# Kernel optimization log

Hardware: AMD Instinct MI355X
Metric: run time of the kernel (lower is better)

Reference implementation:

```python
import jax, jax.numpy as jnp
import numpy as np

NODE_F = 8      # node_features
HID = 128       # hidden_dim
HEADS = 8       # nn.MultiheadAttention num_heads
OUT = 256       # output_dim
MAX_ATOMS = 4096  # max_pocket_atoms
NEIGHBOR_RADIUS = 3.0   # _compute_surface_scores neighbor_radius


def setup_inputs() -> dict:
    key = jax.random.key(0)
    ks = jax.random.split(key, 16)
    N, M = 16384, 32
    x = jax.random.normal(ks[0], (N, NODE_F), dtype=jnp.float32)
    pos = jax.random.normal(ks[1], (N, 3), dtype=jnp.float32) * 10.0
    ligand_pos = jax.random.normal(ks[2], (M, 3), dtype=jnp.float32) * 3.0

    def lin(k, fan_in, fan_out):
        return jax.random.normal(k, (fan_in, fan_out), dtype=jnp.float32) / np.sqrt(fan_in)

    return {
        'x': x, 'pos': pos, 'ligand_pos': ligand_pos,
        'W_node': lin(ks[3], NODE_F, HID), 'b_node': jnp.zeros((HID,), jnp.float32),
        'Wq': lin(ks[4], HID, HID), 'bq': jnp.zeros((HID,), jnp.float32),
        'Wk': lin(ks[5], HID, HID), 'bk': jnp.zeros((HID,), jnp.float32),
        'Wv': lin(ks[6], HID, HID), 'bv': jnp.zeros((HID,), jnp.float32),
        'Wo': lin(ks[7], HID, HID), 'bo': jnp.zeros((HID,), jnp.float32),
        'W1': lin(ks[8], HID, OUT), 'b1': jnp.zeros((OUT,), jnp.float32),
        'W2': lin(ks[9], OUT, OUT), 'b2': jnp.zeros((OUT,), jnp.float32),
    }


def _select_binding_site(pos, ligand_pos, k):
    # select_by_binding_site_proximity: distance-to-ligand-center + surface scores, topk
    lig_center = jnp.mean(ligand_pos, axis=0)                       # [3]
    d_lig = jnp.linalg.norm(pos - lig_center, axis=1)               # [N]
    # _compute_surface_scores: cdist(pos,pos) < 3.0, count neighbors (minus self)
    sq = jnp.sum(pos * pos, axis=1)                                 # [N]
    d2 = sq[:, None] + sq[None, :] - 2.0 * (pos @ pos.T)            # [N,N] squared distances
    neighbor_counts = jnp.sum(d2 < NEIGHBOR_RADIUS ** 2, axis=1) - 1
    surface = 1.0 / (neighbor_counts.astype(jnp.float32) + 1.0)
    scores = 1.0 / (1.0 + d_lig / 5.0) + 0.5 * surface
    _, idx = jax.lax.top_k(scores, k)                               # largest=True
    return idx


def reference(x, pos, ligand_pos, W_node, b_node, Wq, bq, Wk, bk, Wv, bv, Wo, bo, W1, b1, W2, b2):
    # N > max_pocket_atoms -> smart selection (adaptive with ligand_pos => binding_site)
    idx = _select_binding_site(pos, ligand_pos, MAX_ATOMS)
    xs = x[idx]                                                     # [K, NODE_F]

    # node embedding (E3 net call fails in the original -> h = node_embedding(x))
    h = xs @ W_node + b_node                                        # [K, HID]

    # MultiheadAttention over the single (batch=None) sequence, eval mode (no dropout)
    K = MAX_ATOMS
    dh = HID // HEADS
    q = (h @ Wq + bq).reshape(K, HEADS, dh).transpose(1, 0, 2)      # [H,K,dh]
    k_ = (h @ Wk + bk).reshape(K, HEADS, dh).transpose(1, 0, 2)
    v = (h @ Wv + bv).reshape(K, HEADS, dh).transpose(1, 0, 2)
    attn = jax.nn.softmax(jnp.einsum('hqd,hkd->hqk', q, k_) / np.sqrt(dh), axis=-1)
    av = jnp.einsum('hqk,hkd->hqd', attn, v).transpose(1, 0, 2).reshape(K, HID)
    h_att = av @ Wo + bo                                            # [K, HID]

    # global mean pool + output projection (Linear-ReLU-Linear)
    pooled = jnp.mean(h_att, axis=0)                                # [HID]
    out = jax.nn.relu(pooled @ W1 + b1) @ W2 + b2                   # [OUT]
    return out
```

## Files before the change

### kernel.cpp

```cpp
#include <hip/hip_runtime.h>
#include <cstdint>
#include <cstddef>

#define NPTS 16384
#define KSEL 4096
#define HIDDEN 128
#define NHEADS 8
#define DHEAD 16
#define OUTD 256
#define NSLICE 4

typedef __attribute__((ext_vector_type(8))) short bf16x8;
typedef __attribute__((ext_vector_type(4))) float f32x4;

#if defined(__has_builtin)
#if __has_builtin(__builtin_amdgcn_exp2f)
#define E2(x) __builtin_amdgcn_exp2f(x)
#endif
#endif
#ifndef E2
#define E2(x) exp2f(x)
#endif

constexpr size_t OFF_PX  = 1024;
constexpr size_t OFF_PY  = OFF_PX  + (size_t)NPTS*4;
constexpr size_t OFF_PZ  = OFF_PY  + (size_t)NPTS*4;
constexpr size_t OFF_SQ  = OFF_PZ  + (size_t)NPTS*4;
constexpr size_t OFF_DL  = OFF_SQ  + (size_t)NPTS*4;
constexpr size_t OFF_CNT = OFF_DL  + (size_t)NPTS*4;
constexpr size_t OFF_SEL = OFF_CNT + (size_t)NPTS*4;
constexpr size_t SZ_PK   = (size_t)NHEADS*KSEL*32*2;
constexpr size_t OFF_QPK = OFF_SEL + (size_t)KSEL*4;
constexpr size_t OFF_KPK = OFF_QPK + SZ_PK;
constexpr size_t OFF_V   = OFF_KPK + SZ_PK;
constexpr size_t OFF_LP  = OFF_V  + (size_t)KSEL*HIDDEN*4;
constexpr size_t OFF_RL  = OFF_LP + (size_t)NHEADS*KSEL*NSLICE*4;
constexpr size_t OFF_WP  = OFF_RL + (size_t)NHEADS*KSEL*4;
constexpr size_t OFF_PAV = OFF_WP + (size_t)NHEADS*KSEL*NSLICE*4;

__device__ __forceinline__ unsigned short f2bf(float f) {
    union { float f; unsigned u; } v; v.f = f;
    unsigned r = v.u + 0x7fffu + ((v.u >> 16) & 1u);
    return (unsigned short)(r >> 16);
}
__device__ __forceinline__ float bf2f(unsigned short h) {
    union { unsigned u; float f; } v; v.u = ((unsigned)h) << 16;
    return v.f;
}

__global__ void __launch_bounds__(256) k_prep(const float* __restrict__ pos, const float* __restrict__ lig, int M,
                       float* __restrict__ px, float* __restrict__ py, float* __restrict__ pz,
                       float* __restrict__ sq, float* __restrict__ dl) {
    __shared__ float ls[128];
    __shared__ float ctr[3];
    int tid = threadIdx.x;
    for (int i = tid; i < 3 * M; i += 256) ls[i] = lig[i];
    __syncthreads();
    if (tid < 3) {
        float s = 0.f;
        for (int i = 0; i < M; i++) s += ls[i * 3 + tid];
        ctr[tid] = s / (float)M;
    }
    __syncthreads();
    int i = blockIdx.x * 256 + tid;
    float x = pos[i*3+0], y = pos[i*3+1], z = pos[i*3+2];
    px[i] = x; py[i] = y; pz[i] = z;
    sq[i] = (x*x + y*y) + z*z;
    float dx = x - ctr[0], dy = y - ctr[1], dz = z - ctr[2];
    dl[i] = sqrtf((dx*dx + dy*dy) + dz*dz);
}

__global__ void __launch_bounds__(256) k_neighbor(const float* __restrict__ px, const float* __restrict__ py,
                                                  const float* __restrict__ pz, const float* __restrict__ sq,
                                                  int* __restrict__ cnt) {
    __shared__ float4 xt[128], yt[128], zt[128], st[128];
    int tid = threadIdx.x;
    int i = blockIdx.x * 256 + tid;
    float xi = px[i], yi = py[i], zi = pz[i], si = sq[i];
    int jbase = blockIdx.y * 512;
    if (tid < 128) {
        xt[tid] = ((const float4*)(px + jbase))[tid];
        yt[tid] = ((const float4*)(py + jbase))[tid];
        zt[tid] = ((const float4*)(pz + jbase))[tid];
        st[tid] = ((const float4*)(sq + jbase))[tid];
    }
    __syncthreads();
    int c = 0;
    for (int t = 0; t < 128; t++) {
        float4 xj = xt[t], yj = yt[t], zj = zt[t], sj = st[t];
        { float dot = fmaf(xi, xj.x, fmaf(yi, yj.x, zi*zj.x)); float d2 = (si + sj.x) - 2.0f*dot; c += (d2 < 9.0f); }
        { float dot = fmaf(xi, xj.y, fmaf(yi, yj.y, zi*zj.y)); float d2 = (si + sj.y) - 2.0f*dot; c += (d2 < 9.0f); }
        { float dot = fmaf(xi, xj.z, fmaf(yi, yj.z, zi*zj.z)); float d2 = (si + sj.z) - 2.0f*dot; c += (d2 < 9.0f); }
        { float dot = fmaf(xi, xj.w, fmaf(yi, yj.w, zi*zj.w)); float d2 = (si + sj.w) - 2.0f*dot; c += (d2 < 9.0f); }
    }
    atomicAdd(&cnt[i], c);
}

__global__ void __launch_bounds__(1024) k_select(const float* __restrict__ dl, const int* __restrict__ cnt,
                                                 int* __restrict__ sel) {
    __shared__ unsigned int sk[NPTS];
    __shared__ int hist[256];
    __shared__ unsigned int s_prefix;
    __shared__ int s_rem, s_eqtot, s_nout, s_digit, s_cgt;
    int tid = threadIdx.x;
    for (int i = tid; i < NPTS; i += 1024) {
        float score = 1.0f / (1.0f + dl[i] / 5.0f) + 0.5f * (1.0f / (float)cnt[i]);
        unsigned int u = __float_as_uint(score);
        sk[i] = u ^ ((u & 0x80000000u) ? 0xFFFFFFFFu : 0x80000000u);
    }
    if (tid == 0) { s_prefix = 0; s_rem = KSEL; s_nout = 0; s_eqtot = 0; }
    __syncthreads();
    for (int p = 0; p < 4; p++) {
        int sh = 24 - 8 * p;
        if (tid < 256) hist[tid] = 0;
        __syncthreads();
        unsigned int pref = s_prefix;
        int shp = (p == 0) ? 0 : (32 - 8 * p);
        for (int i = tid; i < NPTS; i += 1024) {
            unsigned int key = sk[i];
            bool m = (p == 0) || ((key >> shp) == pref);
            if (m) atomicAdd(&hist[(key >> sh) & 255], 1);
        }
        __syncthreads();
        int rem = s_rem;
        if (tid < 256) {
            int cg = 0;
            for (int d = tid + 1; d < 256; d++) cg += hist[d];
            if (cg < rem && cg + hist[tid] >= rem) { s_digit = tid; s_cgt = cg; }
        }
        __syncthreads();
        if (tid == 0) {
            s_prefix = (s_prefix << 8) | (unsigned int)s_digit;
            s_rem = rem - s_cgt;
            if (p == 3) s_eqtot = hist[s_digit];
        }
        __syncthreads();
    }
    unsigned int T = s_prefix;
    int need_eq = s_rem;
    for (int i = tid; i < NPTS; i += 1024)
        if (sk[i] > T) sel[atomicAdd(&s_nout, 1)] = i;
    __syncthreads();
    if (s_eqtot == need_eq) {
        for (int i = tid; i < NPTS; i += 1024)
            if (sk[i] == T) sel[atomicAdd(&s_nout, 1)] = i;
    } else {
        for (int i = tid; i < NPTS; i += 1024) {
            if (sk[i] == T) {
                int rank = 0;
                for (int j = 0; j < i; j++) rank += (sk[j] == T);
                if (rank < need_eq) sel[atomicAdd(&s_nout, 1)] = i;
            }
        }
    }
}

__device__ __forceinline__ void proj8(const float hs[8][HIDDEN], const float* __restrict__ W,
                                      float b, int d, float* acc) {
    #pragma unroll
    for (int r = 0; r < 8; r++) acc[r] = b;
    for (int c = 0; c < HIDDEN; c += 4) {
        float w0 = W[(c+0)*HIDDEN+d], w1 = W[(c+1)*HIDDEN+d], w2 = W[(c+2)*HIDDEN+d], w3 = W[(c+3)*HIDDEN+d];
        #pragma unroll
        for (int r = 0; r < 8; r++) {
            float4 h4 = *(const float4*)&hs[r][c];
            float a = acc[r];
            a = fmaf(h4.x, w0, a); a = fmaf(h4.y, w1, a); a = fmaf(h4.z, w2, a); a = fmaf(h4.w, w3, a);
            acc[r] = a;
        }
    }
}

__global__ void __launch_bounds__(128) k_qkv(const float* __restrict__ x, const int* __restrict__ sel,
        const float* __restrict__ Wn, const float* __restrict__ bn,
        const float* __restrict__ Wq, const float* __restrict__ bq,
        const float* __restrict__ Wk, const float* __restrict__ bk,
        const float* __restrict__ Wv, const float* __restrict__ bv,
        unsigned short* __restrict__ qpk, unsigned short* __restrict__ kpk,
        float* __restrict__ vg) {
    __shared__ float xs[8][8];
    __shared__ __align__(16) float hs[8][HIDDEN];
    int d = threadIdx.x;
    int r0 = blockIdx.x * 8;
    if (d < 64) { int rr = d >> 3, cc = d & 7; xs[rr][cc] = x[(size_t)sel[r0 + rr] * 8 + cc]; }
    __syncthreads();
    {
        float wn[8];
        #pragma unroll
        for (int c = 0; c < 8; c++) wn[c] = Wn[c * HIDDEN + d];
        float b = bn[d];
        #pragma unroll
        for (int r = 0; r < 8; r++) {
            float a = b;
            #pragma unroll
            for (int c = 0; c < 8; c++) a = fmaf(xs[r][c], wn[c], a);
            hs[r][d] = a;
        }
    }
    __syncthreads();
    int hh = d >> 4, dd = d & 15;
    float acc[8];
    proj8(hs, Wq, bq[d], d, acc);
    #pragma unroll
    for (int r = 0; r < 8; r++) {
        float val = acc[r] * 0.36067376022224085f;
        unsigned short hi = f2bf(val);
        unsigned short lo = f2bf(val - bf2f(hi));
        size_t idx = ((size_t)(hh * KSEL) + r0 + r) * 32 + dd;
        qpk[idx] = hi; qpk[idx + 16] = lo;
    }
    proj8(hs, Wk, bk[d], d, acc);
    #pragma unroll
    for (int r = 0; r < 8; r++) {
        float val = acc[r];
        unsigned short hi = f2bf(val);
        unsigned short lo = f2bf(val - bf2f(hi));
        size_t idx = ((size_t)(hh * KSEL) + r0 + r) * 32 + dd;
        kpk[idx] = hi; kpk[idx + 16] = lo;
    }
    proj8(hs, Wv, bv[d], d, acc);
    #pragma unroll
    for (int r = 0; r < 8; r++) vg[(size_t)(r0+r)*HIDDEN + d] = acc[r];
}

__global__ void __launch_bounds__(256) k_attn_l(
        const unsigned short* __restrict__ qpk, const unsigned short* __restrict__ kpk,
        float* __restrict__ lp) {
    __shared__ unsigned short smem[256 * 40];
    int tid = threadIdx.x;
    int ks = blockIdx.x, yg = blockIdx.y, h = blockIdx.z;
    size_t hb = (size_t)h * KSEL;
    int lane = tid & 63, w = tid >> 6;
    int n = lane & 15, g = lane >> 4;
    int q0w = yg * 64 + w * 16;
    bf16x8 afrag = *(const bf16x8*)(qpk + (hb + q0w + n) * 32 + g * 8);
    float l0 = 0.f, l1 = 0.f, l2 = 0.f, l3 = 0.f;
    int b1off = (g & 1) * 8;
    int b2off = 16 + g * 8;
    for (int kc = 0; kc < 4; kc++) {
        __syncthreads();
        {
            int krow = ks * 1024 + kc * 256 + tid;
            const float4* src = (const float4*)(kpk + (hb + krow) * 32);
            float4 a0 = src[0], a1 = src[1], a2 = src[2], a3 = src[3];
            float4* dst = (float4*)&smem[tid * 40];
            dst[0] = a0; dst[1] = a1; dst[2] = a2; dst[3] = a3;
        }
        __syncthreads();
        #pragma unroll 4
        for (int t = 0; t < 16; t++) {
            const unsigned short* rowp = &smem[(t * 16 + n) * 40];
            bf16x8 b1 = *(const bf16x8*)(rowp + b1off);
            bf16x8 b2 = {0,0,0,0,0,0,0,0};
            if (g < 2) b2 = *(const bf16x8*)(rowp + b2off);
            f32x4 c = {0.f, 0.f, 0.f, 0.f};
            c = __builtin_amdgcn_mfma_f32_16x16x32_bf16(afrag, b1, c, 0, 0, 0);
            c = __builtin_amdgcn_mfma_f32_16x16x32_bf16(afrag, b2, c, 0, 0, 0);
            l0 += E2(c[0]); l1 += E2(c[1]); l2 += E2(c[2]); l3 += E2(c[3]);
        }
    }
    #pragma unroll
    for (int m = 1; m < 16; m <<= 1) {
        l0 += __shfl_xor(l0, m); l1 += __shfl_xor(l1, m);
        l2 += __shfl_xor(l2, m); l3 += __shfl_xor(l3, m);
    }
    if (n == 0) {
        size_t base = (hb + q0w + g * 4) * NSLICE + ks;
        lp[base]            = l0; lp[base + NSLICE]     = l1;
        lp[base + 2*NSLICE] = l2; lp[base + 3*NSLICE]   = l3;
    }
}

__global__ void k_rl(const float* __restrict__ lp, float* __restrict__ rl) {
    int i = blockIdx.x * 256 + threadIdx.x;
    float4 p = ((const float4*)lp)[i];
    rl[i] = 1.0f / ((p.x + p.y) + (p.z + p.w));
}

__global__ void __launch_bounds__(256) k_attn_w(
        const unsigned short* __restrict__ qpk, const unsigned short* __restrict__ kpk,
        const float* __restrict__ rl, float* __restrict__ wp) {
    __shared__ unsigned short smem[256 * 40];
    __shared__ float rls[256];
    int tid = threadIdx.x;
    int qs = blockIdx.x, yg = blockIdx.y, h = blockIdx.z;
    size_t hb = (size_t)h * KSEL;
    int lane = tid & 63, w = tid >> 6;
    int n = lane & 15, g = lane >> 4;
    int j0w = yg * 64 + w * 16;
    bf16x8 afrag = *(const bf16x8*)(kpk + (hb + j0w + n) * 32 + g * 8);
    float w0 = 0.f, w1 = 0.f, w2 = 0.f, w3 = 0.f;
    int b1off = (g & 1) * 8;
    int b2off = 16 + g * 8;
    for (int qc = 0; qc < 4; qc++) {
        __syncthreads();
        {
            int qrow = qs * 1024 + qc * 256 + tid;
            const float4* src = (const float4*)(qpk + (hb + qrow) * 32);
            float4 a0 = src[0], a1 = src[1], a2 = src[2], a3 = src[3];
            float4* dst = (float4*)&smem[tid * 40];
            dst[0] = a0; dst[1] = a1; dst[2] = a2; dst[3] = a3;
            rls[tid] = rl[hb + qrow];
        }
        __syncthreads();
        #pragma unroll 4
        for (int t = 0; t < 16; t++) {
            const unsigned short* rowp = &smem[(t * 16 + n) * 40];
            bf16x8 b1 = *(const bf16x8*)(rowp + b1off);
            bf16x8 b2 = {0,0,0,0,0,0,0,0};
            if (g < 2) b2 = *(const bf16x8*)(rowp + b2off);
            f32x4 c = {0.f, 0.f, 0.f, 0.f};
            c = __builtin_amdgcn_mfma_f32_16x16x32_bf16(afrag, b1, c, 0, 0, 0);
            c = __builtin_amdgcn_mfma_f32_16x16x32_bf16(afrag, b2, c, 0, 0, 0);
            float rv = rls[t * 16 + n];
            w0 = fmaf(E2(c[0]), rv, w0); w1 = fmaf(E2(c[1]), rv, w1);
            w2 = fmaf(E2(c[2]), rv, w2); w3 = fmaf(E2(c[3]), rv, w3);
        }
    }
    #pragma unroll
    for (int m = 1; m < 16; m <<= 1) {
        w0 += __shfl_xor(w0, m); w1 += __shfl_xor(w1, m);
        w2 += __shfl_xor(w2, m); w3 += __shfl_xor(w3, m);
    }
    if (n == 0) {
        size_t base = (hb + j0w + g * 4) * NSLICE + qs;
        wp[base]            = w0; wp[base + NSLICE]     = w1;
        wp[base + 2*NSLICE] = w2; wp[base + 3*NSLICE]   = w3;
    }
}

__global__ void __launch_bounds__(256) k_colsum(const float* __restrict__ wp, const float* __restrict__ vg,
                                                float* __restrict__ pav) {
    __shared__ float wl[NHEADS][128];
    __shared__ float red[128];
    int tid = threadIdx.x;
    int jb = blockIdx.x * 128;
    for (int i = tid; i < NHEADS * 128; i += 256) {
        int h = i >> 7, jl = i & 127;
        float4 p = ((const float4*)wp)[(size_t)h * KSEL + jb + jl];
        wl[h][jl] = (p.x + p.y) + (p.z + p.w);
    }
    __syncthreads();
    int d = tid & 127, g = tid >> 7;
    int h = d >> 4;
    float acc = 0.f;
    for (int jl = g * 64; jl < g * 64 + 64; jl++)
        acc = fmaf(wl[h][jl], vg[(size_t)(jb + jl) * HIDDEN + d], acc);
    if (g == 1) red[d] = acc;
    __syncthreads();
    if (g == 0) atomicAdd(&pav[d], (acc + red[d]) * (1.0f / (float)KSEL));
}

__global__ void __launch_bounds__(256) k_final(const float* __restrict__ pav,
        const float* __restrict__ Wo, const float* __restrict__ bo,
        const float* __restrict__ W1, const float* __restrict__ b1,
        const float* __restrict__ W2, const float* __restrict__ b2,
        float* __restrict__ out) {
    __shared__ float sp[HIDDEN];
    __shared__ float st[OUTD];
    int t = threadIdx.x;
    if (t < HIDDEN) {
        float a = bo[t];
        for (int c = 0; c < HIDDEN; c++) a = fmaf(pav[c], Wo[c * HIDDEN + t], a);
        sp[t] = a;
    }
    __syncthreads();
    {
        float a = b1[t];
        for (int c = 0; c < HIDDEN; c++) a = fmaf(sp[c], W1[c * OUTD + t], a);
        st[t] = fmaxf(a, 0.f);
    }
    __syncthreads();
    {
        float o = b2[t];
        for (int c = 0; c < OUTD; c++) o = fmaf(st[c], W2[c * OUTD + t], o);
        out[t] = o;
    }
}

extern "C" void kernel_launch(void* const* d_in, const int* in_sizes, int n_in,
                              void* d_out, int out_size, void* d_ws, size_t ws_size,
                              hipStream_t stream) {
    (void)n_in; (void)out_size; (void)ws_size;
    const float* x   = (const float*)d_in[0];
    const float* pos = (const float*)d_in[1];
    const float* lig = (const float*)d_in[2];
    const float* Wn  = (const float*)d_in[3];
    const float* bn  = (const float*)d_in[4];
    const float* Wq  = (const float*)d_in[5];
    const float* bq  = (const float*)d_in[6];
    const float* Wk  = (const float*)d_in[7];
    const float* bk  = (const float*)d_in[8];
    const float* Wv  = (const float*)d_in[9];
    const float* bv  = (const float*)d_in[10];
    const float* Wo  = (const float*)d_in[11];
    const float* bo  = (const float*)d_in[12];
    const float* W1  = (const float*)d_in[13];
    const float* b1  = (const float*)d_in[14];
    const float* W2  = (const float*)d_in[15];
    const float* b2  = (const float*)d_in[16];
    int M = in_sizes[2] / 3;

    char* ws = (char*)d_ws;
    float*          px  = (float*)(ws + OFF_PX);
    float*          py  = (float*)(ws + OFF_PY);
    float*          pz  = (float*)(ws + OFF_PZ);
    float*          sq  = (float*)(ws + OFF_SQ);
    float*          dl  = (float*)(ws + OFF_DL);
    int*            cnt = (int*)  (ws + OFF_CNT);
    int*            sel = (int*)  (ws + OFF_SEL);
    unsigned short* qpk = (unsigned short*)(ws + OFF_QPK);
    unsigned short* kpk = (unsigned short*)(ws + OFF_KPK);
    float*          vg  = (float*)(ws + OFF_V);
    float*          lp  = (float*)(ws + OFF_LP);
    float*          rl  = (float*)(ws + OFF_RL);
    float*          wp  = (float*)(ws + OFF_WP);
    float*          pav = (float*)(ws + OFF_PAV);

    hipMemsetAsync(ws + OFF_CNT, 0, (size_t)NPTS * 4, stream);
    hipMemsetAsync(ws + OFF_PAV, 0, (size_t)HIDDEN * 4, stream);

    hipLaunchKernelGGL(k_prep,     dim3(64),       dim3(256),  0, stream, pos, lig, M, px, py, pz, sq, dl);
    hipLaunchKernelGGL(k_neighbor, dim3(64, 32),   dim3(256),  0, stream, px, py, pz, sq, cnt);
    hipLaunchKernelGGL(k_select,   dim3(1),        dim3(1024), 0, stream, dl, cnt, sel);
    hipLaunchKernelGGL(k_qkv,      dim3(KSEL/8),   dim3(128),  0, stream, x, sel, Wn, bn, Wq, bq, Wk, bk, Wv, bv, qpk, kpk, vg);
    hipLaunchKernelGGL(k_attn_l,   dim3(4, 64, 8), dim3(256),  0, stream, qpk, kpk, lp);
    hipLaunchKernelGGL(k_rl,       dim3(NHEADS*KSEL/256), dim3(256), 0, stream, lp, rl);
    hipLaunchKernelGGL(k_attn_w,   dim3(4, 64, 8), dim3(256),  0, stream, qpk, kpk, rl, wp);
    hipLaunchKernelGGL(k_colsum,   dim3(32),       dim3(256),  0, stream, wp, vg, pav);
    hipLaunchKernelGGL(k_final,    dim3(1),        dim3(256),  0, stream, pav, Wo, bo, W1, b1, W2, b2, (float*)d_out);
}
```

Before: 289.7 us.

## Compute pairwise neighbor counts with bf16 split MFMA plus exact fixup

Replaces the scalar FP32 all-pairs distance loop with MFMA 16x16x32 bf16 products, using a hi/lo bf16 split of coordinates to approximate -2·dot plus the squared norms. Pairs whose approximate distance lies within an error band of the radius threshold are appended to a flag list, and a new fixup kernel recomputes them exactly in FP32. The top-k digit search in the select kernel also swaps its per-thread O(256) suffix sum for a parallel scan. The risks are atomic contention on the flag counter and silent miscounts if more than the capped number of pairs are flagged or the error band is too tight.

```diff
diff --git a/kernel.cpp b/kernel.cpp
--- a/kernel.cpp
+++ b/kernel.cpp
@@ -9,6 +9,7 @@
 #define DHEAD 16
 #define OUTD 256
 #define NSLICE 4
+#define FCAP 131072
 
 typedef __attribute__((ext_vector_type(8))) short bf16x8;
 typedef __attribute__((ext_vector_type(4))) float f32x4;
@@ -22,21 +23,22 @@
 #define E2(x) exp2f(x)
 #endif
 
-constexpr size_t OFF_PX  = 1024;
-constexpr size_t OFF_PY  = OFF_PX  + (size_t)NPTS*4;
-constexpr size_t OFF_PZ  = OFF_PY  + (size_t)NPTS*4;
-constexpr size_t OFF_SQ  = OFF_PZ  + (size_t)NPTS*4;
-constexpr size_t OFF_DL  = OFF_SQ  + (size_t)NPTS*4;
-constexpr size_t OFF_CNT = OFF_DL  + (size_t)NPTS*4;
-constexpr size_t OFF_SEL = OFF_CNT + (size_t)NPTS*4;
-constexpr size_t SZ_PK   = (size_t)NHEADS*KSEL*32*2;
-constexpr size_t OFF_QPK = OFF_SEL + (size_t)KSEL*4;
-constexpr size_t OFF_KPK = OFF_QPK + SZ_PK;
-constexpr size_t OFF_V   = OFF_KPK + SZ_PK;
-constexpr size_t OFF_LP  = OFF_V  + (size_t)KSEL*HIDDEN*4;
-constexpr size_t OFF_RL  = OFF_LP + (size_t)NHEADS*KSEL*NSLICE*4;
-constexpr size_t OFF_WP  = OFF_RL + (size_t)NHEADS*KSEL*4;
-constexpr size_t OFF_PAV = OFF_WP + (size_t)NHEADS*KSEL*NSLICE*4;
+constexpr size_t OFF_PA    = 1024;
+constexpr size_t OFF_PB    = OFF_PA  + (size_t)NPTS*32;
+constexpr size_t OFF_SQ    = OFF_PB  + (size_t)NPTS*32;
+constexpr size_t OFF_DL    = OFF_SQ  + (size_t)NPTS*4;
+constexpr size_t OFF_CNT   = OFF_DL  + (size_t)NPTS*4;
+constexpr size_t OFF_NFLAG = OFF_CNT + (size_t)NPTS*4;
+constexpr size_t OFF_FLG   = OFF_NFLAG + 1024;
+constexpr size_t OFF_SEL   = OFF_FLG + (size_t)FCAP*4;
+constexpr size_t SZ_PK     = (size_t)NHEADS*KSEL*32*2;
+constexpr size_t OFF_QPK   = OFF_SEL + (size_t)KSEL*4;
+constexpr size_t OFF_KPK   = OFF_QPK + SZ_PK;
+constexpr size_t OFF_V     = OFF_KPK + SZ_PK;
+constexpr size_t OFF_LP    = OFF_V  + (size_t)KSEL*HIDDEN*4;
+constexpr size_t OFF_RL    = OFF_LP + (size_t)NHEADS*KSEL*NSLICE*4;
+constexpr size_t OFF_WP    = OFF_RL + (size_t)NHEADS*KSEL*4;
+constexpr size_t OFF_PAV   = OFF_WP + (size_t)NHEADS*KSEL*NSLICE*4;
 
 __device__ __forceinline__ unsigned short f2bf(float f) {
     union { float f; unsigned u; } v; v.f = f;
@@ -49,7 +51,7 @@
 }
 
 __global__ void __launch_bounds__(256) k_prep(const float* __restrict__ pos, const float* __restrict__ lig, int M,
-                       float* __restrict__ px, float* __restrict__ py, float* __restrict__ pz,
+                       unsigned short* __restrict__ pa, unsigned short* __restrict__ pb,
                        float* __restrict__ sq, float* __restrict__ dl) {
     __shared__ float ls[128];
     __shared__ float ctr[3];
@@ -64,42 +66,113 @@
     __syncthreads();
     int i = blockIdx.x * 256 + tid;
     float x = pos[i*3+0], y = pos[i*3+1], z = pos[i*3+2];
-    px[i] = x; py[i] = y; pz[i] = z;
     sq[i] = (x*x + y*y) + z*z;
     float dx = x - ctr[0], dy = y - ctr[1], dz = z - ctr[2];
     dl[i] = sqrtf((dx*dx + dy*dy) + dz*dz);
-}
-
-__global__ void __launch_bounds__(256) k_neighbor(const float* __restrict__ px, const float* __restrict__ py,
-                                                  const float* __restrict__ pz, const float* __restrict__ sq,
-                                                  int* __restrict__ cnt) {
-    __shared__ float4 xt[128], yt[128], zt[128], st[128];
+    unsigned short xh = f2bf(x); float xr = bf2f(xh); float xl = x - xr;
+    unsigned short yh = f2bf(y); float yr = bf2f(yh); float yl = y - yr;
+    unsigned short zh = f2bf(z); float zr = bf2f(zh); float zl = z - zr;
+    unsigned short xlb = f2bf(xl), ylb = f2bf(yl), zlb = f2bf(zl);
+    unsigned short xhA = f2bf(-2.f*xr), xlA = f2bf(-2.f*xl);
+    unsigned short yhA = f2bf(-2.f*yr), ylA = f2bf(-2.f*yl);
+    unsigned short zhA = f2bf(-2.f*zr), zlA = f2bf(-2.f*zl);
+    union { unsigned short s[16]; float4 f[2]; } A, B;
+    #pragma unroll
+    for (int t = 0; t < 16; t++) { A.s[t] = 0; B.s[t] = 0; }
+    A.s[0]=xhA; A.s[1]=xhA; A.s[2]=xlA;
+    A.s[3]=yhA; A.s[4]=yhA; A.s[5]=ylA;
+    A.s[6]=zhA; A.s[7]=zhA; A.s[8]=zlA;
+    A.s[9]=xlA; A.s[10]=ylA; A.s[11]=zlA;
+    B.s[0]=xh;  B.s[1]=xlb;  B.s[2]=xh;
+    B.s[3]=yh;  B.s[4]=ylb;  B.s[5]=yh;
+    B.s[6]=zh;  B.s[7]=zlb;  B.s[8]=zh;
+    B.s[9]=xlb; B.s[10]=ylb; B.s[11]=zlb;
+    float4* pad = (float4*)(pa + (size_t)i * 16);
+    pad[0] = A.f[0]; pad[1] = A.f[1];
+    float4* pbd = (float4*)(pb + (size_t)i * 16);
+    pbd[0] = B.f[0]; pbd[1] = B.f[1];
+}
+
+__global__ void __launch_bounds__(256) k_neighbor(
+        const unsigned short* __restrict__ pa, const unsigned short* __restrict__ pb,
+        const float* __restrict__ sq, int* __restrict__ cnt,
+        unsigned int* __restrict__ flg, unsigned int* __restrict__ nflag) {
+    __shared__ unsigned short bs[256 * 24];
+    __shared__ float sjs[256];
     int tid = threadIdx.x;
-    int i = blockIdx.x * 256 + tid;
-    float xi = px[i], yi = py[i], zi = pz[i], si = sq[i];
-    int jbase = blockIdx.y * 512;
-    if (tid < 128) {
-        xt[tid] = ((const float4*)(px + jbase))[tid];
-        yt[tid] = ((const float4*)(py + jbase))[tid];
-        zt[tid] = ((const float4*)(pz + jbase))[tid];
-        st[tid] = ((const float4*)(sq + jbase))[tid];
-    }
-    __syncthreads();
-    int c = 0;
-    for (int t = 0; t < 128; t++) {
-        float4 xj = xt[t], yj = yt[t], zj = zt[t], sj = st[t];
-        { float dot = fmaf(xi, xj.x, fmaf(yi, yj.x, zi*zj.x)); float d2 = (si + sj.x) - 2.0f*dot; c += (d2 < 9.0f); }
-        { float dot = fmaf(xi, xj.y, fmaf(yi, yj.y, zi*zj.y)); float d2 = (si + sj.y) - 2.0f*dot; c += (d2 < 9.0f); }
-        { float dot = fmaf(xi, xj.z, fmaf(yi, yj.z, zi*zj.z)); float d2 = (si + sj.z) - 2.0f*dot; c += (d2 < 9.0f); }
-        { float dot = fmaf(xi, xj.w, fmaf(yi, yj.w, zi*zj.w)); float d2 = (si + sj.w) - 2.0f*dot; c += (d2 < 9.0f); }
-    }
-    atomicAdd(&cnt[i], c);
+    int lane = tid & 63, w = tid >> 6;
+    int n = lane & 15, g = lane >> 4;
+    int i0 = blockIdx.x * 64 + w * 16;
+    bf16x8 afrag = {0,0,0,0,0,0,0,0};
+    if (g < 2) afrag = *(const bf16x8*)(pa + (size_t)(i0 + n) * 16 + g * 8);
+    int irow = i0 + g * 4;
+    float si0 = sq[irow+0], si1 = sq[irow+1], si2 = sq[irow+2], si3 = sq[irow+3];
+    int boff = (g < 2) ? g * 8 : 0;
+    int jb0 = blockIdx.y * 4096;
+    int c0 = 0, c1 = 0, c2 = 0, c3 = 0;
+    for (int ch = 0; ch < 16; ch++) {
+        __syncthreads();
+        int jb = jb0 + ch * 256;
+        {
+            const float4* src = (const float4*)(pb + (size_t)(jb + tid) * 16);
+            float4 v0 = src[0], v1 = src[1];
+            float4* dst = (float4*)&bs[tid * 24];
+            dst[0] = v0; dst[1] = v1;
+            sjs[tid] = sq[jb + tid];
+        }
+        __syncthreads();
+        #pragma unroll 4
+        for (int t = 0; t < 16; t++) {
+            int jj = t * 16 + n;
+            bf16x8 bfrag = *(const bf16x8*)&bs[jj * 24 + boff];
+            float sj = sjs[jj];
+            float s0 = si0 + sj, s1 = si1 + sj, s2 = si2 + sj, s3 = si3 + sj;
+            f32x4 c; c[0] = s0; c[1] = s1; c[2] = s2; c[3] = s3;
+            c = __builtin_amdgcn_mfma_f32_16x16x32_bf16(afrag, bfrag, c, 0, 0, 0);
+            float t0 = fmaf(s0, 3.0e-4f, 0.01f), t1 = fmaf(s1, 3.0e-4f, 0.01f);
+            float t2 = fmaf(s2, 3.0e-4f, 0.01f), t3 = fmaf(s3, 3.0e-4f, 0.01f);
+            float d0 = c[0] - 9.0f, d1 = c[1] - 9.0f, d2_ = c[2] - 9.0f, d3 = c[3] - 9.0f;
+            c0 += (d0 < -t0); c1 += (d1 < -t1); c2 += (d2_ < -t2); c3 += (d3 < -t3);
+            int j = jb + jj;
+            if (fabsf(d0) < t0) { unsigned idx = atomicAdd(nflag, 1u); if (idx < FCAP) flg[idx] = ((unsigned)(irow+0) << 14) | (unsigned)j; }
+            if (fabsf(d1) < t1) { unsigned idx = atomicAdd(nflag, 1u); if (idx < FCAP) flg[idx] = ((unsigned)(irow+1) << 14) | (unsigned)j; }
+            if (fabsf(d2_) < t2) { unsigned idx = atomicAdd(nflag, 1u); if (idx < FCAP) flg[idx] = ((unsigned)(irow+2) << 14) | (unsigned)j; }
+            if (fabsf(d3) < t3) { unsigned idx = atomicAdd(nflag, 1u); if (idx < FCAP) flg[idx] = ((unsigned)(irow+3) << 14) | (unsigned)j; }
+        }
+    }
+    #pragma unroll
+    for (int m = 1; m < 16; m <<= 1) {
+        c0 += __shfl_xor(c0, m); c1 += __shfl_xor(c1, m);
+        c2 += __shfl_xor(c2, m); c3 += __shfl_xor(c3, m);
+    }
+    if (n == 0) {
+        atomicAdd(&cnt[irow+0], c0);
+        atomicAdd(&cnt[irow+1], c1);
+        atomicAdd(&cnt[irow+2], c2);
+        atomicAdd(&cnt[irow+3], c3);
+    }
+}
+
+__global__ void __launch_bounds__(256) k_fixup(const float* __restrict__ pos, const float* __restrict__ sq,
+        const unsigned int* __restrict__ flg, const unsigned int* __restrict__ nflag,
+        int* __restrict__ cnt) {
+    int nf = (int)*nflag; if (nf > FCAP) nf = FCAP;
+    for (int idx = blockIdx.x * 256 + threadIdx.x; idx < nf; idx += gridDim.x * 256) {
+        unsigned pr = flg[idx];
+        int i = (int)(pr >> 14), j = (int)(pr & 16383u);
+        float xi = pos[i*3+0], yi = pos[i*3+1], zi = pos[i*3+2];
+        float xj = pos[j*3+0], yj = pos[j*3+1], zj = pos[j*3+2];
+        float dot = fmaf(xi, xj, fmaf(yi, yj, zi * zj));
+        float d2 = (sq[i] + sq[j]) - 2.0f * dot;
+        if (d2 < 9.0f) atomicAdd(&cnt[i], 1);
+    }
 }
 
 __global__ void __launch_bounds__(1024) k_select(const float* __restrict__ dl, const int* __restrict__ cnt,
                                                  int* __restrict__ sel) {
     __shared__ unsigned int sk[NPTS];
     __shared__ int hist[256];
+    __shared__ int scan2[256];
     __shared__ unsigned int s_prefix;
     __shared__ int s_rem, s_eqtot, s_nout, s_digit, s_cgt;
     int tid = threadIdx.x;
@@ -122,11 +195,20 @@
             if (m) atomicAdd(&hist[(key >> sh) & 255], 1);
         }
         __syncthreads();
+        if (tid < 256) scan2[tid] = hist[tid];
+        __syncthreads();
+        for (int off = 1; off < 256; off <<= 1) {
+            int v = 0;
+            if (tid < 256) { v = scan2[tid]; if (tid + off < 256) v += scan2[tid + off]; }
+            __syncthreads();
+            if (tid < 256) scan2[tid] = v;
+            __syncthreads();
+        }
         int rem = s_rem;
         if (tid < 256) {
-            int cg = 0;
-            for (int d = tid + 1; d < 256; d++) cg += hist[d];
-            if (cg < rem && cg + hist[tid] >= rem) { s_digit = tid; s_cgt = cg; }
+            int hi = scan2[tid];
+            int lo = hi - hist[tid];
+            if (hi >= rem && lo < rem) { s_digit = tid; s_cgt = lo; }
         }
         __syncthreads();
         if (tid == 0) {
@@ -402,12 +484,13 @@
     int M = in_sizes[2] / 3;
 
     char* ws = (char*)d_ws;
-    float*          px  = (float*)(ws + OFF_PX);
-    float*          py  = (float*)(ws + OFF_PY);
-    float*          pz  = (float*)(ws + OFF_PZ);
+    unsigned short* pa  = (unsigned short*)(ws + OFF_PA);
+    unsigned short* pb  = (unsigned short*)(ws + OFF_PB);
     float*          sq  = (float*)(ws + OFF_SQ);
     float*          dl  = (float*)(ws + OFF_DL);
     int*            cnt = (int*)  (ws + OFF_CNT);
+    unsigned int*   nfl = (unsigned int*)(ws + OFF_NFLAG);
+    unsigned int*   flg = (unsigned int*)(ws + OFF_FLG);
     int*            sel = (int*)  (ws + OFF_SEL);
     unsigned short* qpk = (unsigned short*)(ws + OFF_QPK);
     unsigned short* kpk = (unsigned short*)(ws + OFF_KPK);
@@ -417,11 +500,12 @@
     float*          wp  = (float*)(ws + OFF_WP);
     float*          pav = (float*)(ws + OFF_PAV);
 
-    hipMemsetAsync(ws + OFF_CNT, 0, (size_t)NPTS * 4, stream);
+    hipMemsetAsync(ws + OFF_CNT, 0, (size_t)NPTS * 4 + 1024, stream);
     hipMemsetAsync(ws + OFF_PAV, 0, (size_t)HIDDEN * 4, stream);
 
-    hipLaunchKernelGGL(k_prep,     dim3(64),       dim3(256),  0, stream, pos, lig, M, px, py, pz, sq, dl);
-    hipLaunchKernelGGL(k_neighbor, dim3(64, 32),   dim3(256),  0, stream, px, py, pz, sq, cnt);
+    hipLaunchKernelGGL(k_prep,     dim3(64),       dim3(256),  0, stream, pos, lig, M, pa, pb, sq, dl);
+    hipLaunchKernelGGL(k_neighbor, dim3(256, 4),   dim3(256),  0, stream, pa, pb, sq, cnt, flg, nfl);
+    hipLaunchKernelGGL(k_fixup,    dim3(32),       dim3(256),  0, stream, pos, sq, flg, nfl, cnt);
     hipLaunchKernelGGL(k_select,   dim3(1),        dim3(1024), 0, stream, dl, cnt, sel);
     hipLaunchKernelGGL(k_qkv,      dim3(KSEL/8),   dim3(128),  0, stream, x, sel, Wn, bn, Wq, bq, Wk, bk, Wv, bv, qpk, kpk, vg);
     hipLaunchKernelGGL(k_attn_l,   dim3(4, 64, 8), dim3(256),  0, stream, qpk, kpk, lp);
```

Result: slower. 506.3 us (+74.8%).
